# Kernel tuning notes

Measured on AMD Instinct MI355X. Metric: run time of the kernel, lower is better.

The kernel has to match this reference:

```python
import jax, jax.numpy as jnp
import numpy as np

N_BINS = 32
EPS = 6.4 / 256.0
LO = -3.2 - EPS / 2.0
HI = 3.2 - EPS / 2.0
BIN_W = (HI - LO) / N_BINS


def _rgb_uv_hist_one(img):
    # img: [3, H, W] -> [3, 32, 32] sqrt-normalized RGB-uv histogram
    C, H, W = img.shape
    # cv2 INTER_NEAREST downsample: src index = floor(dst * scale)
    ry = jnp.floor(jnp.arange(N_BINS) * (H / N_BINS)).astype(jnp.int32)
    rx = jnp.floor(jnp.arange(N_BINS) * (W / N_BINS)).astype(jnp.int32)
    small = img[:, ry][:, :, rx]                 # [3, 32, 32]
    px = small.reshape(3, -1)                    # [3, 1024]
    valid = jnp.all(px > 0, axis=0)              # pixels with all channels > 0
    Iy = jnp.sqrt(jnp.sum(px * px, axis=0))      # per-pixel L2 norm (weights)
    w = jnp.where(valid, Iy, 0.0)
    px_safe = jnp.where(px > 0, px, 1.0)         # guard log for masked pixels
    logs = jnp.log(px_safe)                      # [3, 1024]
    hists = []
    for i in range(3):
        r = [j for j in range(3) if j != i]
        Iu = logs[i] - logs[r[1]]
        Iv = logs[i] - logs[r[0]]
        inb = valid & (Iu >= LO) & (Iu <= HI) & (Iv >= LO) & (Iv <= HI)
        iu = jnp.clip(jnp.floor((Iu - LO) / BIN_W).astype(jnp.int32), 0, N_BINS - 1)
        iv = jnp.clip(jnp.floor((Iv - LO) / BIN_W).astype(jnp.int32), 0, N_BINS - 1)
        flat = iu * N_BINS + iv                  # histogram2d: rows=Iu, cols=Iv
        h = jnp.zeros(N_BINS * N_BINS, dtype=px.dtype).at[flat].add(jnp.where(inb, w, 0.0))
        h = h / jnp.sum(h)
        hists.append(jnp.sqrt(h).reshape(N_BINS, N_BINS))
    return jnp.stack(hists)                      # [3, 32, 32]


def setup_inputs() -> dict:
    key = jax.random.key(0)
    ks = jax.random.split(key, 7)
    B, H, W = 32, 512, 512
    inp_img = jax.random.uniform(ks[0], (B, 3, H, W), dtype=jnp.float32)
    s = 0.02
    return {
        "inp_img": inp_img,
        "W1": jax.random.normal(ks[1], (1024, 3072), jnp.float32) * s,
        "b1": jax.random.normal(ks[2], (1024,), jnp.float32) * s,
        "W2": jax.random.normal(ks[3], (512, 1024), jnp.float32) * s,
        "b2": jax.random.normal(ks[4], (512,), jnp.float32) * s,
        "W3": jax.random.normal(ks[5], (256, 512), jnp.float32) * s,
        "b3": jax.random.normal(ks[6], (256,), jnp.float32) * s,
    }


def reference(inp_img, W1, b1, W2, b2, W3, b3):
    B = inp_img.shape[0]
    hist = jax.vmap(_rgb_uv_hist_one)(inp_img).reshape(B, -1)  # [B, 3072]
    hist = jax.lax.stop_gradient(hist)  # original code detaches the histogram
    x = jax.nn.relu(hist @ W1.T + b1)
    x = jax.nn.relu(x @ W2.T + b2)
    x = jax.nn.relu(x @ W3.T + b3)      # [B, 256]
    return x[..., None, None]            # [B, 256, 1, 1]
```

## Files before the change

### kernel.cpp

```cpp
#include <hip/hip_runtime.h>
#include <math.h>

#define IMG_H 512
#define IMG_W 512
#define HWSZ (IMG_H * IMG_W)
#define BATCH 32

__global__ __launch_bounds__(256) void hist_part_k(const float* __restrict__ img,
                                                   float* __restrict__ hp)
{
    const int img_i = blockIdx.x >> 2;
    const int blk   = blockIdx.x & 3;
    const int tid   = threadIdx.x;

    __shared__ float hh[3072];
    for (int i = tid; i < 3072; i += 256) hh[i] = 0.f;
    __syncthreads();

    const int p  = blk * 256 + tid;
    const int py = p >> 5;
    const int px = p & 31;
    const size_t base = (size_t)img_i * 3 * HWSZ + (size_t)(py * 16) * IMG_W + (size_t)(px * 16);

    const float r  = img[base];
    const float g  = img[base + HWSZ];
    const float bl = img[base + 2 * HWSZ];

    const bool valid = (r > 0.f) && (g > 0.f) && (bl > 0.f);

    const float LOc = (float)(-3.2 - (6.4 / 256.0) * 0.5);
    const float HIc = (float)( 3.2 - (6.4 / 256.0) * 0.5);
    const float BWc = (float)(((3.2 - (6.4 / 256.0) * 0.5) - (-3.2 - (6.4 / 256.0) * 0.5)) / 32.0);

    if (valid) {
        const float w  = sqrtf(r * r + g * g + bl * bl);
        const float lr = logf(r);
        const float lg = logf(g);
        const float lb = logf(bl);

        float us[3] = { lr - lb, lg - lb, lb - lg };
        float vs[3] = { lr - lg, lg - lr, lb - lr };

        #pragma unroll
        for (int i = 0; i < 3; ++i) {
            const float U = us[i];
            const float V = vs[i];
            if (U >= LOc && U <= HIc && V >= LOc && V <= HIc) {
                int iu = (int)floorf((U - LOc) / BWc); iu = iu < 31 ? iu : 31;
                int iv = (int)floorf((V - LOc) / BWc); iv = iv < 31 ? iv : 31;
                atomicAdd(&hh[i * 1024 + iu * 32 + iv], w);
            }
        }
    }
    __syncthreads();

    float* outp = hp + (size_t)blockIdx.x * 3072;
    for (int i = tid; i < 3072; i += 256) outp[i] = hh[i];
}

__global__ __launch_bounds__(1024) void hist_norm_k(const float* __restrict__ hp,
                                                    float* __restrict__ histT)
{
    const int img_i = blockIdx.x;
    const int tid   = threadIdx.x;
    const int wid   = tid >> 6;
    const int lane  = tid & 63;

    __shared__ float red[17];
    const float* base = hp + (size_t)img_i * 4 * 3072;

    #pragma unroll
    for (int c = 0; c < 3; ++c) {
        const int idx = c * 1024 + tid;
        float v = base[idx] + base[3072 + idx] + base[2 * 3072 + idx] + base[3 * 3072 + idx];

        float t = v;
        #pragma unroll
        for (int off = 32; off; off >>= 1) t += __shfl_down(t, off);
        if (lane == 0) red[wid] = t;
        __syncthreads();
        if (tid == 0) {
            float s = 0.f;
            #pragma unroll
            for (int j = 0; j < 16; ++j) s += red[j];
            red[16] = s;
        }
        __syncthreads();
        const float s = red[16];
        histT[(size_t)(c * 1024 + tid) * BATCH + img_i] = sqrtf(v / s);
        __syncthreads();
    }
}

template <int K, int N, int S>
__global__ __launch_bounds__(256) void gemm_part_k(const float* __restrict__ xT,
                                                   const float* __restrict__ W,
                                                   float* __restrict__ part)
{
    constexpr int C  = K / S;
    constexpr int NG = N / 8;

    const int wave = (blockIdx.x * 256 + threadIdx.x) >> 6;
    const int lane = threadIdx.x & 63;
    const int og   = wave % NG;
    const int s    = wave / NG;
    const int o0   = og * 8;
    const int k0   = s * C;
    const int khalf = lane >> 5;
    const int b     = lane & 31;

    float acc[8] = {0.f, 0.f, 0.f, 0.f, 0.f, 0.f, 0.f, 0.f};

    const float* xp = xT + (size_t)k0 * BATCH + lane;

    #pragma unroll 4
    for (int kk = 0; kk < C; kk += 2) {
        const float xv = xp[kk * BATCH];
        const int k = k0 + kk + khalf;
        #pragma unroll
        for (int j = 0; j < 8; ++j)
            acc[j] += xv * W[(o0 + j) * K + k];
    }

    #pragma unroll
    for (int j = 0; j < 8; ++j)
        acc[j] += __shfl_xor(acc[j], 32);

    if (khalf == 0) {
        float* pp = part + ((size_t)s * N + o0) * BATCH + b;
        #pragma unroll
        for (int j = 0; j < 8; ++j)
            pp[j * BATCH] = acc[j];
    }
}

template <int N, int S, bool LAST>
__global__ __launch_bounds__(256) void reduce_bias_relu_k(const float* __restrict__ part,
                                                          const float* __restrict__ bias,
                                                          float* __restrict__ out)
{
    const int t = blockIdx.x * 256 + threadIdx.x;
    float s = 0.f;
    #pragma unroll
    for (int i = 0; i < S; ++i)
        s += part[(size_t)i * N * BATCH + t];

    const int o = t >> 5;
    const int b = t & 31;
    s += bias[o];
    s = fmaxf(s, 0.f);
    if (LAST)
        out[b * N + o] = s;
    else
        out[t] = s;
}

extern "C" void kernel_launch(void* const* d_in, const int* in_sizes, int n_in,
                              void* d_out, int out_size, void* d_ws, size_t ws_size,
                              hipStream_t stream)
{
    const float* img = (const float*)d_in[0];
    const float* W1  = (const float*)d_in[1];
    const float* b1  = (const float*)d_in[2];
    const float* W2  = (const float*)d_in[3];
    const float* b2  = (const float*)d_in[4];
    const float* W3  = (const float*)d_in[5];
    const float* b3  = (const float*)d_in[6];
    float* out = (float*)d_out;

    float* ws = (float*)d_ws;
    float* histT   = ws;
    float* x1T     = histT + 3072 * BATCH;
    float* x2T     = x1T   + 1024 * BATCH;
    float* scratch = x2T   + 512 * BATCH;

    hist_part_k<<<BATCH * 4, 256, 0, stream>>>(img, scratch);
    hist_norm_k<<<BATCH, 1024, 0, stream>>>(scratch, histT);

    gemm_part_k<3072, 1024, 16><<<(1024 / 8) * 16 / 4, 256, 0, stream>>>(histT, W1, scratch);
    reduce_bias_relu_k<1024, 16, false><<<1024 * BATCH / 256, 256, 0, stream>>>(scratch, b1, x1T);

    gemm_part_k<1024, 512, 16><<<(512 / 8) * 16 / 4, 256, 0, stream>>>(x1T, W2, scratch);
    reduce_bias_relu_k<512, 16, false><<<512 * BATCH / 256, 256, 0, stream>>>(scratch, b2, x2T);

    gemm_part_k<512, 256, 16><<<(256 / 8) * 16 / 4, 256, 0, stream>>>(x2T, W3, scratch);
    reduce_bias_relu_k<256, 16, true><<<256 * BATCH / 256, 256, 0, stream>>>(scratch, b3, out);
}
```

Baseline: 189.5 us.

## Replace split-K partials and reduce kernels with atomic accumulation into bias-initialized outputs

Each GEMM layer now accumulates its split-K partial sums with atomicAdd straight into an output buffer. The hist kernel pre-fills these buffers with the bias using extra blocks. ReLU moves into the next GEMM's input load and into a small finish kernel, which removes the three reduce kernels and their partial-buffer traffic. Activations use a k-pair interleaved layout so each lane loads a float2 and has no cross-half shuffle, and the weight row offsets are made wave-uniform. The risks are atomic contention and non-deterministic summation order.

```diff
diff --git a/kernel.cpp b/kernel.cpp
--- a/kernel.cpp
+++ b/kernel.cpp
@@ -6,9 +6,36 @@
 #define HWSZ (IMG_H * IMG_W)
 #define BATCH 32
 
+__device__ __forceinline__ size_t xidx(int k, int b) {
+    return (size_t)(k >> 1) * 64 + b * 2 + (k & 1);
+}
+
 __global__ __launch_bounds__(256) void hist_part_k(const float* __restrict__ img,
-                                                   float* __restrict__ hp)
+                                                   float* __restrict__ hp,
+                                                   const float* __restrict__ b1,
+                                                   const float* __restrict__ b2,
+                                                   const float* __restrict__ b3,
+                                                   float* __restrict__ y1,
+                                                   float* __restrict__ y2,
+                                                   float* __restrict__ y3)
 {
+    if (blockIdx.x >= 128) {
+        const int t = (blockIdx.x - 128) * 256 + threadIdx.x;
+        if (t < 32768) {
+            const int o = ((t >> 6) << 1) | (t & 1);
+            y1[t] = b1[o];
+        } else if (t < 49152) {
+            const int u = t - 32768;
+            const int o = ((u >> 6) << 1) | (u & 1);
+            y2[u] = b2[o];
+        } else {
+            const int u = t - 49152;
+            const int o = ((u >> 6) << 1) | (u & 1);
+            y3[u] = b3[o];
+        }
+        return;
+    }
+
     const int img_i = blockIdx.x >> 2;
     const int blk   = blockIdx.x & 3;
     const int tid   = threadIdx.x;
@@ -87,72 +114,58 @@
         }
         __syncthreads();
         const float s = red[16];
-        histT[(size_t)(c * 1024 + tid) * BATCH + img_i] = sqrtf(v / s);
+        histT[xidx(c * 1024 + tid, img_i)] = sqrtf(v / s);
         __syncthreads();
     }
 }
 
-template <int K, int N, int S>
-__global__ __launch_bounds__(256) void gemm_part_k(const float* __restrict__ xT,
-                                                   const float* __restrict__ W,
-                                                   float* __restrict__ part)
+template <int K, int N, int S, bool RELU>
+__global__ __launch_bounds__(256) void gemm_atomic_k(const float* __restrict__ xT,
+                                                     const float* __restrict__ W,
+                                                     float* __restrict__ y)
 {
     constexpr int C  = K / S;
     constexpr int NG = N / 8;
 
     const int wave = (blockIdx.x * 256 + threadIdx.x) >> 6;
     const int lane = threadIdx.x & 63;
-    const int og   = wave % NG;
-    const int s    = wave / NG;
-    const int o0   = og * 8;
-    const int k0   = s * C;
-    const int khalf = lane >> 5;
-    const int b     = lane & 31;
+    const int b    = lane & 31;
+    const int o0   = __builtin_amdgcn_readfirstlane((wave % NG) * 8);
+    const int k0   = __builtin_amdgcn_readfirstlane((wave / NG) * C);
+
+    const float* Wr[8];
+    #pragma unroll
+    for (int j = 0; j < 8; ++j) Wr[j] = W + (size_t)(o0 + j) * K + k0;
+
+    const float2* xp = reinterpret_cast<const float2*>(xT + (size_t)k0 * BATCH) + b;
 
     float acc[8] = {0.f, 0.f, 0.f, 0.f, 0.f, 0.f, 0.f, 0.f};
 
-    const float* xp = xT + (size_t)k0 * BATCH + lane;
+    #pragma unroll 4
+    for (int kk2 = 0; kk2 < C / 2; ++kk2) {
+        float2 v = xp[kk2 * BATCH];
+        if (RELU) { v.x = fmaxf(v.x, 0.f); v.y = fmaxf(v.y, 0.f); }
+        #pragma unroll
+        for (int j = 0; j < 8; ++j) {
+            acc[j] = fmaf(v.x, Wr[j][2 * kk2],     acc[j]);
+            acc[j] = fmaf(v.y, Wr[j][2 * kk2 + 1], acc[j]);
+        }
+    }
 
-    #pragma unroll 4
-    for (int kk = 0; kk < C; kk += 2) {
-        const float xv = xp[kk * BATCH];
-        const int k = k0 + kk + khalf;
+    if (lane < 32) {
         #pragma unroll
         for (int j = 0; j < 8; ++j)
-            acc[j] += xv * W[(o0 + j) * K + k];
-    }
-
-    #pragma unroll
-    for (int j = 0; j < 8; ++j)
-        acc[j] += __shfl_xor(acc[j], 32);
-
-    if (khalf == 0) {
-        float* pp = part + ((size_t)s * N + o0) * BATCH + b;
-        #pragma unroll
-        for (int j = 0; j < 8; ++j)
-            pp[j * BATCH] = acc[j];
+            atomicAdd(&y[xidx(o0 + j, b)], acc[j]);
     }
 }
 
-template <int N, int S, bool LAST>
-__global__ __launch_bounds__(256) void reduce_bias_relu_k(const float* __restrict__ part,
-                                                          const float* __restrict__ bias,
-                                                          float* __restrict__ out)
+__global__ __launch_bounds__(256) void finish_k(const float* __restrict__ y3,
+                                                float* __restrict__ out)
 {
     const int t = blockIdx.x * 256 + threadIdx.x;
-    float s = 0.f;
-    #pragma unroll
-    for (int i = 0; i < S; ++i)
-        s += part[(size_t)i * N * BATCH + t];
-
-    const int o = t >> 5;
-    const int b = t & 31;
-    s += bias[o];
-    s = fmaxf(s, 0.f);
-    if (LAST)
-        out[b * N + o] = s;
-    else
-        out[t] = s;
+    const int b = t >> 8;
+    const int o = t & 255;
+    out[t] = fmaxf(y3[xidx(o, b)], 0.f);
 }
 
 extern "C" void kernel_launch(void* const* d_in, const int* in_sizes, int n_in,
@@ -169,20 +182,18 @@
     float* out = (float*)d_out;
 
     float* ws = (float*)d_ws;
-    float* histT   = ws;
-    float* x1T     = histT + 3072 * BATCH;
-    float* x2T     = x1T   + 1024 * BATCH;
-    float* scratch = x2T   + 512 * BATCH;
+    float* hp    = ws;
+    float* histT = hp    + 128 * 3072;
+    float* y1    = histT + 3072 * BATCH;
+    float* y2    = y1    + 1024 * BATCH;
+    float* y3    = y2    +  512 * BATCH;
 
-    hist_part_k<<<BATCH * 4, 256, 0, stream>>>(img, scratch);
-    hist_norm_k<<<BATCH, 1024, 0, stream>>>(scratch, histT);
+    hist_part_k<<<128 + 224, 256, 0, stream>>>(img, hp, b1, b2, b3, y1, y2, y3);
+    hist_norm_k<<<BATCH, 1024, 0, stream>>>(hp, histT);
 
-    gemm_part_k<3072, 1024, 16><<<(1024 / 8) * 16 / 4, 256, 0, stream>>>(histT, W1, scratch);
-    reduce_bias_relu_k<1024, 16, false><<<1024 * BATCH / 256, 256, 0, stream>>>(scratch, b1, x1T);
+    gemm_atomic_k<3072, 1024, 16, false><<<512, 256, 0, stream>>>(histT, W1, y1);
+    gemm_atomic_k<1024,  512, 16, true ><<<256, 256, 0, stream>>>(y1, W2, y2);
+    gemm_atomic_k< 512,  256, 16, true ><<<128, 256, 0, stream>>>(y2, W3, y3);
 
-    gemm_part_k<1024, 512, 16><<<(512 / 8) * 16 / 4, 256, 0, stream>>>(x1T, W2, scratch);
-    reduce_bias_relu_k<512, 16, false><<<512 * BATCH / 256, 256, 0, stream>>>(scratch, b2, x2T);
-
-    gemm_part_k<512, 256, 16><<<(256 / 8) * 16 / 4, 256, 0, stream>>>(x2T, W3, scratch);
-    reduce_bias_relu_k<256, 16, true><<<256 * BATCH / 256, 256, 0, stream>>>(scratch, b3, out);
+    finish_k<<<32, 256, 0, stream>>>(y3, out);
 }
```

Result: no change. 188.6 us (-0.5%).
